# Kernel tuning notes

Measured on AMD Instinct MI355X. Metric: run time of the kernel, lower is better.

Reference implementation:

```python
import jax, jax.numpy as jnp
import numpy as np

ALPHA = 4.0  # spikingjelly default Sigmoid surrogate alpha
BN_EPS = 1e-5

@jax.custom_vjp
def spike(x):
    return (x >= 0.0).astype(x.dtype)

def _spike_fwd(x):
    return spike(x), x

def _spike_bwd(res, g):
    s = jax.nn.sigmoid(ALPHA * res)
    return (g * ALPHA * s * (1.0 - s),)

spike.defvjp(_spike_fwd, _spike_bwd)

def lif(x, tau=2.0, vth=1.0):
    # MultiStepLIFNode: hard reset (v_reset=0), detach_reset=True, scan over time axis 0
    def step(v, xt):
        h = v + (xt - v) / tau          # charge
        s = spike(h - vth)              # fire (surrogate grad)
        v_next = h * (1.0 - jax.lax.stop_gradient(s))  # detached hard reset to 0
        return v_next, s
    _, out = jax.lax.scan(step, jnp.zeros_like(x[0]), x)
    return out

def conv_bn(x, w, b, g, be, m, var):
    # x: [TB, C, N]; 1x1 Conv1d is a channel GEMM, then eval-mode BatchNorm1d
    y = jnp.einsum('oc,bcn->bon', w, x) + b[None, :, None]
    inv = g / jnp.sqrt(var + BN_EPS)
    return (y - m[None, :, None]) * inv[None, :, None] + be[None, :, None]

def setup_inputs() -> dict:
    key = jax.random.key(0)
    T, B, C, H, W = 4, 32, 512, 14, 14
    ks = jax.random.split(key, 32)
    d = {'x': jax.random.normal(ks[0], (T, B, C, H, W), dtype=jnp.float32)}
    scale = 1.0 / np.sqrt(C)
    i = 1
    for p in ['q', 'k', 'v', 'p']:
        d[p + '_cw'] = jax.random.normal(ks[i], (C, C), dtype=jnp.float32) * scale; i += 1
        d[p + '_cb'] = jax.random.normal(ks[i], (C,), dtype=jnp.float32) * 0.1; i += 1
        d[p + '_bg'] = jnp.ones((C,), dtype=jnp.float32)
        d[p + '_bb'] = jnp.zeros((C,), dtype=jnp.float32)
        d[p + '_bm'] = jax.random.normal(ks[i], (C,), dtype=jnp.float32) * 0.1; i += 1
        d[p + '_bv'] = jax.random.uniform(ks[i], (C,), dtype=jnp.float32, minval=0.5, maxval=1.5); i += 1
    d['push_w'] = jnp.asarray(1.0, dtype=jnp.float32)
    d['pull_w'] = jnp.asarray(1.0, dtype=jnp.float32)
    d['pp_bias'] = jnp.asarray(0.0, dtype=jnp.float32)
    return d

def reference(x,
              q_cw, q_cb, q_bg, q_bb, q_bm, q_bv,
              k_cw, k_cb, k_bg, k_bb, k_bm, k_bv,
              v_cw, v_cb, v_bg, v_bb, v_bm, v_bv,
              p_cw, p_cb, p_bg, p_bb, p_bm, p_bv,
              push_w, pull_w, pp_bias):
    T, B, C, H, W = x.shape
    N = H * W
    nh = 8
    hd = C // nh
    scale = 0.125

    xs = lif(x)                                   # head_lif, [T,B,C,H,W]
    xf = xs.reshape(T * B, C, N)
    q = conv_bn(xf, q_cw, q_cb, q_bg, q_bb, q_bm, q_bv).reshape(T, B, C, N)
    k = conv_bn(xf, k_cw, k_cb, k_bg, k_bb, k_bm, k_bv).reshape(T, B, C, N)
    v = conv_bn(xf, v_cw, v_cb, v_bg, v_bb, v_bm, v_bv).reshape(T, B, C, N)

    q_on = lif(q)
    q_off = lif(-q)

    def to_heads(t):  # [T,B,C,N] -> [T,B,nh,N,hd]
        return jnp.swapaxes(t, -1, -2).reshape(T, B, N, nh, hd).transpose(0, 1, 3, 2, 4)

    q_on_h = to_heads(q_on)
    q_off_h = to_heads(q_off)
    k_h = to_heads(lif(k))
    v_h = to_heads(lif(v))

    pw = jax.nn.softplus(push_w)
    pl = jax.nn.softplus(pull_w)
    diff = pw * q_on_h - pl * q_off_h + pp_bias   # push-pull gating
    q_pp = lif(diff)

    kv = jnp.einsum('tbhnd,tbhne->tbhde', k_h, v_h)      # k^T @ v, [T,B,h,hd,hd]
    o = jnp.einsum('tbhnd,tbhde->tbhne', q_pp, kv) * scale

    o = o.transpose(0, 1, 2, 4, 3).reshape(T, B, C, N)   # transpose(3,4) then merge heads
    o = lif(o, vth=0.5)                                   # attn_lif
    o = conv_bn(o.reshape(T * B, C, N), p_cw, p_cb, p_bg, p_bb, p_bm, p_bv)
    return o.reshape(T, B, C, H, W)
```

## Files before the change

kernel.cpp:

```cpp
#include <hip/hip_runtime.h>
#include <hip/hip_bf16.h>
#include <math.h>

typedef unsigned short u16;
typedef unsigned int   u32;

#define CC 512
#define NN 196
#define TT 4
#define BB 32
#define TBB 128
#define NHH 8
#define HD 64

#define ROWS_T  6272
#define CSTRIDE ((size_t)ROWS_T * CC)

typedef __attribute__((ext_vector_type(8))) _Float16 f16x8;
typedef __attribute__((ext_vector_type(4))) float f32x4;

#define ONE_H 0x3C00

__device__ __forceinline__ u16 h_bits(_Float16 h) { return *(u16*)&h; }
__device__ __forceinline__ float h2f(u16 u) { return (float)(*(const _Float16*)&u); }
__device__ __forceinline__ u32 pk2(u16 a, u16 b) { return (u32)a | ((u32)b << 16); }

__device__ __forceinline__ void gld16(const void* g, void* l) {
    __builtin_amdgcn_global_load_lds(
        (const __attribute__((address_space(1))) void*)g,
        (__attribute__((address_space(3))) void*)l, 16, 0, 0);
}

__global__ __launch_bounds__(256) void k_prep(
    const float* __restrict__ qw, const float* __restrict__ kw,
    const float* __restrict__ vw, const float* __restrict__ pw,
    const float* __restrict__ cb0, const float* __restrict__ bg0, const float* __restrict__ bb0,
    const float* __restrict__ bm0, const float* __restrict__ bv0,
    const float* __restrict__ cb1, const float* __restrict__ bg1, const float* __restrict__ bb1,
    const float* __restrict__ bm1, const float* __restrict__ bv1,
    const float* __restrict__ cb2, const float* __restrict__ bg2, const float* __restrict__ bb2,
    const float* __restrict__ bm2, const float* __restrict__ bv2,
    const float* __restrict__ cb3, const float* __restrict__ bg3, const float* __restrict__ bb3,
    const float* __restrict__ bm3, const float* __restrict__ bv3,
    u16* __restrict__ W2, float* __restrict__ SS, float* __restrict__ SH) {
    if (blockIdx.x < 4096) {
        size_t idx = (size_t)blockIdx.x * 256 + threadIdx.x;
        int g = (int)(idx >> 18);
        size_t rem = idx & 262143;
        const float* Ws = (g == 0) ? qw : (g == 1) ? kw : (g == 2) ? vw : pw;
        float w  = Ws[rem];
        _Float16 h0 = (fabsf(w) < 6.2e-5f) ? (_Float16)0.0f : (_Float16)w;
        float r = (w - (float)h0) * 2048.0f;
        _Float16 h1 = (_Float16)r;
        size_t base = (size_t)g * 524288 + rem;
        W2[base] = h_bits(h0); W2[base + 262144] = h_bits(h1);
        return;
    }
    int idx = (blockIdx.x - 4096) * 256 + threadIdx.x;
    int g = idx >> 9, o = idx & 511;
    const float* cb = g == 0 ? cb0 : g == 1 ? cb1 : g == 2 ? cb2 : cb3;
    const float* bg = g == 0 ? bg0 : g == 1 ? bg1 : g == 2 ? bg2 : bg3;
    const float* bb = g == 0 ? bb0 : g == 1 ? bb1 : g == 2 ? bb2 : bb3;
    const float* bm = g == 0 ? bm0 : g == 1 ? bm1 : g == 2 ? bm2 : bm3;
    const float* bv = g == 0 ? bv0 : g == 1 ? bv1 : g == 2 ? bv2 : bv3;
    float inv = bg[o] / sqrtf(bv[o] + 1e-5f);
    SS[g * 512 + o] = inv;
    SH[g * 512 + o] = (cb[o] - bm[o]) * inv + bb[o];
}

__global__ __launch_bounds__(256) void k_head_lif(const float* __restrict__ x, u16* __restrict__ XS) {
    __shared__ float T[64][65];
    const int tid = threadIdx.x;
    const int n0 = blockIdx.x * 64;
    const int b  = blockIdx.y;
    const int c_base = blockIdx.z * 64;
    const int c_l = tid >> 4;
    const int n4  = (tid & 15) * 4;
    const bool lv = (n0 + n4) < NN;
    const int n_r = tid >> 2;
    const int cq  = (tid & 3) * 16;
    const bool wv = (n0 + n_r) < NN;

    float v[4][4];
    #pragma unroll
    for (int k = 0; k < 4; ++k)
        #pragma unroll
        for (int j = 0; j < 4; ++j) v[k][j] = 0.f;

    for (int t = 0; t < TT; ++t) {
        const size_t xb = ((size_t)(t * BB + b) * CC + c_base) * NN;
        float s[4][4];
        #pragma unroll
        for (int k = 0; k < 4; ++k) {
            const int c = c_l + 16 * k;
            float4 xv = make_float4(0.f, 0.f, 0.f, 0.f);
            if (lv) xv = *(const float4*)(x + xb + (size_t)c * NN + n0 + n4);
            float xa[4] = {xv.x, xv.y, xv.z, xv.w};
            #pragma unroll
            for (int j = 0; j < 4; ++j) {
                float h = v[k][j] + (xa[j] - v[k][j]) * 0.5f;
                s[k][j] = (h >= 1.f) ? 1.f : 0.f;
                v[k][j] = (h >= 1.f) ? 0.f : h;
            }
        }
        __syncthreads();
        #pragma unroll
        for (int k = 0; k < 4; ++k)
            #pragma unroll
            for (int j = 0; j < 4; ++j) T[c_l + 16 * k][n4 + j] = s[k][j];
        __syncthreads();
        if (wv) {
            const size_t ob = ((size_t)(t * BB + b) * NN + n0 + n_r) * CC + c_base + cq;
            u16 u[16];
            #pragma unroll
            for (int m = 0; m < 16; ++m) u[m] = (T[cq + m][n_r] != 0.f) ? ONE_H : 0;
            uint4 q0 = make_uint4(pk2(u[0],u[1]),  pk2(u[2],u[3]),  pk2(u[4],u[5]),  pk2(u[6],u[7]));
            uint4 q1 = make_uint4(pk2(u[8],u[9]),  pk2(u[10],u[11]),pk2(u[12],u[13]),pk2(u[14],u[15]));
            *(uint4*)(XS + ob)     = q0;
            *(uint4*)(XS + ob + 8) = q1;
        }
        __syncthreads();
    }
}

__global__ __launch_bounds__(256) void k_gemm_qkv(const u16* __restrict__ S, const u16* __restrict__ W2,
                                                  const float* __restrict__ scale, const float* __restrict__ shift,
                                                  u16* __restrict__ QS, u16* __restrict__ KS, u16* __restrict__ VS,
                                                  const float* __restrict__ PW, const float* __restrict__ PL,
                                                  const float* __restrict__ PB) {
    __shared__ __align__(16) u16 smem[24576];
    u16* Xt  = smem;
    u16* WtF = smem + 8192;
    const int tid  = threadIdx.x;
    const int lane = tid & 63;
    const int w    = tid >> 6;
    const int bid  = blockIdx.x;
    const int work = (bid & 7) * 294 + (bid >> 3);
    const int rrt  = work / 12;
    const int gw   = work - rrt * 12;
    const int g    = gw >> 2;
    const int wtile = gw & 3;
    const int rr0  = rrt * 32;
    const u16* Wb = W2 + (size_t)g * 524288 + (size_t)(wtile * 128) * CC;
    const float* scl = scale + g * 512;
    const float* shf = shift + g * 512;

    const int lrow8  = lane >> 3;
    const int gchunk = ((lane & 7) ^ lrow8) * 8;
    const int l15 = lane & 15;
    const int q4  = lane >> 4;
    const int wm = (w >> 1) * 64, wn = (w & 1) * 64;

    const size_t arow0 = (size_t)w * CSTRIDE + (size_t)rr0 * CC;

    f32x4 acc[4][4];
    f32x4 zz = {0.f, 0.f, 0.f, 0.f};
    #pragma unroll
    for (int i = 0; i < 4; ++i)
        #pragma unroll
        for (int j = 0; j < 4; ++j) acc[i][j] = zz;

    for (int c0 = 0; c0 < CC; c0 += 64) {
        __syncthreads();
        #pragma unroll
        for (int i = 0; i < 4; ++i) {
            int p = w * 4 + i;
            gld16(S + arow0 + (size_t)(i * 8 + lrow8) * CC + c0 + gchunk, &Xt[p * 512]);
        }
        #pragma unroll
        for (int i = 0; i < 8; ++i) {
            int lin = w * 8 + i;
            int s = lin >> 4, p = lin & 15;
            gld16(Wb + (size_t)s * 262144 + (size_t)(p * 8 + lrow8) * CC + c0 + gchunk,
                  WtF + s * 8192 + p * 512);
        }
        __syncthreads();

        #pragma unroll
        for (int ks = 0; ks < 2; ++ks) {
            const int cpo = ((ks * 4 + q4) ^ (l15 & 7)) * 8;
            f16x8 sf[4], sflo[4];
            #pragma unroll
            for (int i = 0; i < 4; ++i) {
                sf[i]   = *(const f16x8*)&Xt[(wm + i * 16 + l15) * 64 + cpo];
                sflo[i] = sf[i] * (_Float16)0.00048828125f;
            }
            #pragma unroll
            for (int s = 0; s < 2; ++s) {
                f16x8 wf[4];
                #pragma unroll
                for (int i = 0; i < 4; ++i)
                    wf[i] = *(const f16x8*)&WtF[s * 8192 + (wn + i * 16 + l15) * 64 + cpo];
                #pragma unroll
                for (int mt = 0; mt < 4; ++mt)
                    #pragma unroll
                    for (int nt = 0; nt < 4; ++nt)
                        acc[mt][nt] = __builtin_amdgcn_mfma_f32_16x16x32_f16(
                            s ? sflo[mt] : sf[mt], wf[nt], acc[mt][nt], 0, 0, 0);
            }
        }
    }

    const float pwv = (g == 0) ? log1pf(expf(PW[0])) : 0.f;
    const float plv = (g == 0) ? log1pf(expf(PL[0])) : 0.f;
    const float pbv = (g == 0) ? PB[0] : 0.f;
    u16* OUT = (g == 0) ? QS : (g == 1) ? KS : VS;
    float* LY = (float*)smem;
    const int pairid = w & 1;
    const int pr  = tid >> 7;
    const int idx = tid & 127;

    #pragma unroll
    for (int cc = 0; cc < 2; ++cc) {
        __syncthreads();
        #pragma unroll
        for (int ntl = 0; ntl < 2; ++ntl) {
            const int nt = cc * 2 + ntl;
            const int o  = wtile * 128 + wn + nt * 16 + l15;
            const float sc = scl[o], sh = shf[o];
            const int col32 = ntl * 16 + l15;
            #pragma unroll
            for (int mt = 0; mt < 4; ++mt) {
                const int tr0 = wm + mt * 16 + q4 * 4;
                #pragma unroll
                for (int r = 0; r < 4; ++r)
                    LY[(pairid * 128 + tr0 + r) * 33 + col32] = acc[mt][nt][r] * sc + sh;
            }
        }
        __syncthreads();
        #pragma unroll
        for (int stp = 0; stp < 4; ++stp) {
            const int chain = stp * 128 + idx;
            const int nn  = chain >> 4;
            const int c2  = (chain & 15) * 2;
            const int rr  = rr0 + nn;
            const float* Lp = &LY[(pr * 128 + nn) * 33 + c2];
            float ya[4][2];
            #pragma unroll
            for (int t = 0; t < 4; ++t) {
                ya[t][0] = Lp[t * 32 * 33];
                ya[t][1] = Lp[t * 32 * 33 + 1];
            }
            const int ocol = wtile * 128 + pr * 64 + cc * 32 + c2;
            u32* op = (u32*)(OUT + (size_t)rr * CC + ocol);
            if (g == 0) {
                float von[2] = {0.f, 0.f}, voff[2] = {0.f, 0.f}, vpp[2] = {0.f, 0.f};
                #pragma unroll
                for (int t = 0; t < 4; ++t) {
                    u16 sp2[2];
                    #pragma unroll
                    for (int j = 0; j < 2; ++j) {
                        float qv = ya[t][j], h;
                        h = von[j]  + ( qv - von[j] ) * 0.5f; bool s1 = (h >= 1.f); von[j]  = s1 ? 0.f : h;
                        h = voff[j] + (-qv - voff[j]) * 0.5f; bool s2 = (h >= 1.f); voff[j] = s2 ? 0.f : h;
                        float diff = pwv * (s1 ? 1.f : 0.f) - plv * (s2 ? 1.f : 0.f) + pbv;
                        h = vpp[j] + (diff - vpp[j]) * 0.5f; bool sp = (h >= 1.f); vpp[j] = sp ? 0.f : h;
                        sp2[j] = sp ? ONE_H : 0;
                    }
                    op[t * (CSTRIDE / 2)] = pk2(sp2[0], sp2[1]);
                }
            } else {
                float vm[2] = {0.f, 0.f};
                #pragma unroll
                for (int t = 0; t < 4; ++t) {
                    u16 s2[2];
                    #pragma unroll
                    for (int j = 0; j < 2; ++j) {
                        float h = vm[j] + (ya[t][j] - vm[j]) * 0.5f;
                        bool s = (h >= 1.f); vm[j] = s ? 0.f : h;
                        s2[j] = s ? ONE_H : 0;
                    }
                    op[t * (CSTRIDE / 2)] = pk2(s2[0], s2[1]);
                }
            }
        }
    }
}

__global__ __launch_bounds__(256) void k_attn(const u16* __restrict__ Q, const u16* __restrict__ K,
                                              const u16* __restrict__ V, u16* __restrict__ OS) {
    __shared__ __align__(16) u16 sm[19584];
    u16* Kt  = sm;
    u16* Vt  = sm + 8704;
    u16* Qs  = sm;
    u16* kvT = sm + 14976;

    const int tid = threadIdx.x;
    const int tb  = blockIdx.x >> 3;
    const int h   = blockIdx.x & 7;
    const size_t gb = (size_t)tb * NN * CC + (size_t)h * HD;

    const int srow = tid >> 2;
    const int sdq  = (tid & 3) * 16;

    const int lane = tid & 63;
    const int w    = tid >> 6;
    const int l15  = lane & 15;
    const int kb8  = (lane >> 4) * 8;
    const int quad = (lane >> 4) * 4;
    const int dh = (w >> 1) * 32, eh = (w & 1) * 32;

    f32x4 accA[2][2];
    f32x4 zz = {0.f, 0.f, 0.f, 0.f};
    #pragma unroll
    for (int i = 0; i < 2; ++i)
        #pragma unroll
        for (int j = 0; j < 2; ++j) accA[i][j] = zz;

    const uint4 z4 = make_uint4(0, 0, 0, 0);

    #pragma unroll
    for (int ch = 0; ch < 2; ++ch) {
        if (ch) __syncthreads();
        #pragma unroll
        for (int c = 0; c < 2; ++c) {
            int n  = ch * 128 + c * 64 + srow;
            int nl = c * 64 + srow;
            bool valid = n < NN;
            const u16* kr = K + gb + (size_t)n * CC + sdq;
            const u16* vr = V + gb + (size_t)n * CC + sdq;
            uint4 ka  = valid ? *(const uint4*)kr : z4;
            uint4 kb2 = valid ? *(const uint4*)(kr + 8) : z4;
            uint4 va  = valid ? *(const uint4*)vr : z4;
            uint4 vb2 = valid ? *(const uint4*)(vr + 8) : z4;
            u32 kwv[8] = {ka.x, ka.y, ka.z, ka.w, kb2.x, kb2.y, kb2.z, kb2.w};
            u32 vwv[8] = {va.x, va.y, va.z, va.w, vb2.x, vb2.y, vb2.z, vb2.w};
            #pragma unroll
            for (int i = 0; i < 8; ++i) {
                Kt[(sdq + 2 * i) * 136 + nl]     = (u16)(kwv[i] & 0xFFFF);
                Kt[(sdq + 2 * i + 1) * 136 + nl] = (u16)(kwv[i] >> 16);
                Vt[(sdq + 2 * i) * 136 + nl]     = (u16)(vwv[i] & 0xFFFF);
                Vt[(sdq + 2 * i + 1) * 136 + nl] = (u16)(vwv[i] >> 16);
            }
        }
        __syncthreads();
        #pragma unroll
        for (int k0 = 0; k0 < 128; k0 += 32) {
            f16x8 af[2], bv[2];
            #pragma unroll
            for (int i = 0; i < 2; ++i) {
                af[i] = *(const f16x8*)&Kt[(dh + i * 16 + l15) * 136 + k0 + kb8];
                bv[i] = *(const f16x8*)&Vt[(eh + i * 16 + l15) * 136 + k0 + kb8];
            }
            #pragma unroll
            for (int i = 0; i < 2; ++i)
                #pragma unroll
                for (int j = 0; j < 2; ++j)
                    accA[i][j] = __builtin_amdgcn_mfma_f32_16x16x32_f16(af[i], bv[j], accA[i][j], 0, 0, 0);
        }
    }
    __syncthreads();

    #pragma unroll
    for (int i = 0; i < 2; ++i)
        #pragma unroll
        for (int j = 0; j < 2; ++j)
            #pragma unroll
            for (int r = 0; r < 4; ++r) {
                int e = eh + j * 16 + l15;
                int d = dh + i * 16 + quad + r;
                _Float16 hv = (_Float16)accA[i][j][r];
                kvT[e * 72 + d] = h_bits(hv);
            }
    #pragma unroll
    for (int p = 0; p < 4; ++p) {
        int n = p * 64 + srow;
        if (n < 208) {
            if (n < NN) {
                const u16* qr = Q + gb + (size_t)n * CC + sdq;
                uint4 qa  = *(const uint4*)qr;
                uint4 qb2 = *(const uint4*)(qr + 8);
                u32 qwv[8] = {qa.x, qa.y, qa.z, qa.w, qb2.x, qb2.y, qb2.z, qb2.w};
                #pragma unroll
                for (int i = 0; i < 8; ++i) {
                    Qs[n * 72 + sdq + 2 * i]     = (u16)(qwv[i] & 0xFFFF);
                    Qs[n * 72 + sdq + 2 * i + 1] = (u16)(qwv[i] >> 16);
                }
            } else {
                #pragma unroll
                for (int i = 0; i < 16; ++i) Qs[n * 72 + sdq + i] = 0;
            }
        }
    }
    __syncthreads();

    f16x8 bq0 = *(const f16x8*)&kvT[(w * 16 + l15) * 72 + 0  + kb8];
    f16x8 bq1 = *(const f16x8*)&kvT[(w * 16 + l15) * 72 + 32 + kb8];
    u16* ob = OS + (size_t)tb * NN * CC + (size_t)h * HD + w * 16 + l15;
    #pragma unroll
    for (int nt = 0; nt < 13; ++nt) {
        f32x4 acc = zz;
        f16x8 a0 = *(const f16x8*)&Qs[(nt * 16 + l15) * 72 + 0  + kb8];
        f16x8 a1 = *(const f16x8*)&Qs[(nt * 16 + l15) * 72 + 32 + kb8];
        acc = __builtin_amdgcn_mfma_f32_16x16x32_f16(a0, bq0, acc, 0, 0, 0);
        acc = __builtin_amdgcn_mfma_f32_16x16x32_f16(a1, bq1, acc, 0, 0, 0);
        #pragma unroll
        for (int r = 0; r < 4; ++r) {
            int n = nt * 16 + quad + r;
            if (n < NN) {
                _Float16 ov = (_Float16)(acc[r] * 0.125f);
                ob[(size_t)n * CC] = h_bits(ov);
            }
        }
    }
}

__global__ __launch_bounds__(256) void k_attn_lif(uint4* __restrict__ OS) {
    const size_t idx = (size_t)blockIdx.x * 256 + threadIdx.x;
    float v[8];
    #pragma unroll
    for (int j = 0; j < 8; ++j) v[j] = 0.f;
    #pragma unroll
    for (int t = 0; t < TT; ++t) {
        const size_t o8 = idx + (size_t)t * (CSTRIDE / 8);
        uint4 d = OS[o8];
        u32 dw[4] = {d.x, d.y, d.z, d.w};
        u16 u[8];
        #pragma unroll
        for (int p = 0; p < 4; ++p) {
            #pragma unroll
            for (int hf = 0; hf < 2; ++hf) {
                int j = p * 2 + hf;
                u16 raw = hf ? (u16)(dw[p] >> 16) : (u16)(dw[p] & 0xFFFF);
                float xv = h2f(raw);
                float h = v[j] + (xv - v[j]) * 0.5f;
                bool s = (h >= 0.5f);
                v[j] = s ? 0.f : h;
                u[j] = s ? ONE_H : 0;
            }
        }
        OS[o8] = make_uint4(pk2(u[0],u[1]), pk2(u[2],u[3]), pk2(u[4],u[5]), pk2(u[6],u[7]));
    }
}

__global__ __launch_bounds__(256) void k_gemm_proj(const u16* __restrict__ S, const u16* __restrict__ W2,
                                                   const float* __restrict__ scale, const float* __restrict__ shift,
                                                   float* __restrict__ Y) {
    __shared__ __align__(16) u16 Xt[128 * 64];
    __shared__ __align__(16) u16 Wt[2][128 * 64];
    const int tid  = threadIdx.x;
    const int lane = tid & 63;
    const int w    = tid >> 6;
    const int bid  = blockIdx.x;
    const int work = (bid & 7) * 98 + (bid >> 3);
    const int ntile = work >> 2;
    const int wtile = work & 3;
    const u16* Sb = S + (size_t)ntile * 128 * CC;
    const u16* Wb = W2 + (size_t)(wtile * 128) * CC;

    const int lrow8  = lane >> 3;
    const int gchunk = ((lane & 7) ^ lrow8) * 8;
    const int l15 = lane & 15;
    const int q4  = lane >> 4;
    const int wm = (w >> 1) * 64, wn = (w & 1) * 64;

    const int tb0 = (ntile * 128) / NN;
    const int bnd = (tb0 + 1) * NN;

    f32x4 acc[4][4];
    f32x4 zz = {0.f, 0.f, 0.f, 0.f};
    #pragma unroll
    for (int i = 0; i < 4; ++i)
        #pragma unroll
        for (int j = 0; j < 4; ++j) acc[i][j] = zz;

    for (int c0 = 0; c0 < CC; c0 += 64) {
        __syncthreads();
        #pragma unroll
        for (int i = 0; i < 4; ++i) {
            int p = w * 4 + i;
            gld16(Sb + (size_t)(p * 8 + lrow8) * CC + c0 + gchunk, &Xt[p * 512]);
        }
        #pragma unroll
        for (int i = 0; i < 8; ++i) {
            int lin = w * 8 + i;
            int s = lin >> 4, p = lin & 15;
            gld16(Wb + (size_t)s * 262144 + (size_t)(p * 8 + lrow8) * CC + c0 + gchunk,
                  &Wt[s][p * 512]);
        }
        __syncthreads();

        #pragma unroll
        for (int ks = 0; ks < 2; ++ks) {
            const int cpo = ((ks * 4 + q4) ^ (l15 & 7)) * 8;
            f16x8 sf[4], sflo[4];
            #pragma unroll
            for (int i = 0; i < 4; ++i) {
                sf[i]   = *(const f16x8*)&Xt[(wn + i * 16 + l15) * 64 + cpo];
                sflo[i] = sf[i] * (_Float16)0.00048828125f;
            }
            #pragma unroll
            for (int s = 0; s < 2; ++s) {
                f16x8 wf[4];
                #pragma unroll
                for (int i = 0; i < 4; ++i)
                    wf[i] = *(const f16x8*)&Wt[s][(wm + i * 16 + l15) * 64 + cpo];
                #pragma unroll
                for (int mt = 0; mt < 4; ++mt)
                    #pragma unroll
                    for (int nt = 0; nt < 4; ++nt)
                        acc[mt][nt] = __builtin_amdgcn_mfma_f32_16x16x32_f16(
                            wf[mt], s ? sflo[nt] : sf[nt], acc[mt][nt], 0, 0, 0);
            }
        }
    }

    #pragma unroll
    for (int mt = 0; mt < 4; ++mt) {
        int o0 = wtile * 128 + wm + mt * 16 + (lane >> 4) * 4;
        #pragma unroll
        for (int nt = 0; nt < 4; ++nt) {
            int row = ntile * 128 + wn + nt * 16 + l15;
            int tb = (row >= bnd) ? tb0 + 1 : tb0;
            int n  = row - tb * NN;
            #pragma unroll
            for (int r = 0; r < 4; ++r)
                Y[((size_t)tb * CC + o0 + r) * NN + n] = acc[mt][nt][r] * scale[o0 + r] + shift[o0 + r];
        }
    }
}

extern "C" void kernel_launch(void* const* d_in, const int* in_sizes, int n_in,
                              void* d_out, int out_size, void* d_ws, size_t ws_size,
                              hipStream_t stream) {
    const float* x    = (const float*)d_in[0];
    const float* q_cw = (const float*)d_in[1];
    const float* q_cb = (const float*)d_in[2];
    const float* q_bg = (const float*)d_in[3];
    const float* q_bb = (const float*)d_in[4];
    const float* q_bm = (const float*)d_in[5];
    const float* q_bv = (const float*)d_in[6];
    const float* k_cw = (const float*)d_in[7];
    const float* k_cb = (const float*)d_in[8];
    const float* k_bg = (const float*)d_in[9];
    const float* k_bb = (const float*)d_in[10];
    const float* k_bm = (const float*)d_in[11];
    const float* k_bv = (const float*)d_in[12];
    const float* v_cw = (const float*)d_in[13];
    const float* v_cb = (const float*)d_in[14];
    const float* v_bg = (const float*)d_in[15];
    const float* v_bb = (const float*)d_in[16];
    const float* v_bm = (const float*)d_in[17];
    const float* v_bv = (const float*)d_in[18];
    const float* p_cw = (const float*)d_in[19];
    const float* p_cb = (const float*)d_in[20];
    const float* p_bg = (const float*)d_in[21];
    const float* p_bb = (const float*)d_in[22];
    const float* p_bm = (const float*)d_in[23];
    const float* p_bv = (const float*)d_in[24];
    const float* pshw = (const float*)d_in[25];
    const float* pllw = (const float*)d_in[26];
    const float* ppb  = (const float*)d_in[27];
    float* out = (float*)d_out;

    if (ws_size < (size_t)242 * 1024 * 1024) return;
    char* W = (char*)d_ws;
    u16*   XS = (u16*)W;
    u16*   QS = (u16*)(W + ((size_t)27 << 20));
    u16*   OS = (u16*)(W + ((size_t)78 << 20));
    u16*   KS = (u16*)(W + ((size_t)182 << 20));
    u16*   VS = (u16*)(W + ((size_t)208 << 20));
    u16*   W2 = (u16*)(W + ((size_t)234 << 20));
    float* SS = (float*)(W + ((size_t)238 << 20));
    float* SH = SS + 2048;

    k_prep<<<4104, 256, 0, stream>>>(q_cw, k_cw, v_cw, p_cw,
                                     q_cb, q_bg, q_bb, q_bm, q_bv,
                                     k_cb, k_bg, k_bb, k_bm, k_bv,
                                     v_cb, v_bg, v_bb, v_bm, v_bv,
                                     p_cb, p_bg, p_bb, p_bm, p_bv, W2, SS, SH);

    k_head_lif<<<dim3(4, 32, 8), 256, 0, stream>>>(x, XS);

    k_gemm_qkv<<<2352, 256, 0, stream>>>(XS, W2, SS, SH, QS, KS, VS, pshw, pllw, ppb);

    k_attn<<<TBB * NHH, 256, 0, stream>>>(QS, KS, VS, OS);
    k_attn_lif<<<1568, 256, 0, stream>>>((uint4*)OS);

    k_gemm_proj<<<784, 256, 0, stream>>>(OS, W2 + 3 * 524288, SS + 1536, SH + 1536, out);
}
```

Baseline: 321.6 us.

## Merge prep and head LIF launches, swizzle K/V LDS tiles, vectorize LDS stores

Merges the weight/BN preparation kernel and the head LIF kernel into one launch by dispatching on block index, which removes one launch and lets the two independent jobs share the GPU. In the attention kernel, the padded K/V transpose tiles are replaced by an XOR-swizzled unpadded layout to cut LDS bank conflicts. The kv tile and Q staging writes are vectorized into packed 64-bit stores instead of 16-bit scalar stores. The fused kernel now always reserves the head LIF shared buffer, which may lower occupancy for the prep blocks.

```diff
diff --git a/kernel.cpp b/kernel.cpp
--- a/kernel.cpp
+++ b/kernel.cpp
@@ -31,7 +31,8 @@
         (__attribute__((address_space(3))) void*)l, 16, 0, 0);
 }
 
-__global__ __launch_bounds__(256) void k_prep(
+__global__ __launch_bounds__(256) void k_prep_head(
+    const float* __restrict__ x, u16* __restrict__ XS,
     const float* __restrict__ qw, const float* __restrict__ kw,
     const float* __restrict__ vw, const float* __restrict__ pw,
     const float* __restrict__ cb0, const float* __restrict__ bg0, const float* __restrict__ bb0,
@@ -43,8 +44,11 @@
     const float* __restrict__ cb3, const float* __restrict__ bg3, const float* __restrict__ bb3,
     const float* __restrict__ bm3, const float* __restrict__ bv3,
     u16* __restrict__ W2, float* __restrict__ SS, float* __restrict__ SH) {
+    __shared__ float T[64][65];
+    const int tid = threadIdx.x;
+
     if (blockIdx.x < 4096) {
-        size_t idx = (size_t)blockIdx.x * 256 + threadIdx.x;
+        size_t idx = (size_t)blockIdx.x * 256 + tid;
         int g = (int)(idx >> 18);
         size_t rem = idx & 262143;
         const float* Ws = (g == 0) ? qw : (g == 1) ? kw : (g == 2) ? vw : pw;
@@ -56,24 +60,24 @@
         W2[base] = h_bits(h0); W2[base + 262144] = h_bits(h1);
         return;
     }
-    int idx = (blockIdx.x - 4096) * 256 + threadIdx.x;
-    int g = idx >> 9, o = idx & 511;
-    const float* cb = g == 0 ? cb0 : g == 1 ? cb1 : g == 2 ? cb2 : cb3;
-    const float* bg = g == 0 ? bg0 : g == 1 ? bg1 : g == 2 ? bg2 : bg3;
-    const float* bb = g == 0 ? bb0 : g == 1 ? bb1 : g == 2 ? bb2 : bb3;
-    const float* bm = g == 0 ? bm0 : g == 1 ? bm1 : g == 2 ? bm2 : bm3;
-    const float* bv = g == 0 ? bv0 : g == 1 ? bv1 : g == 2 ? bv2 : bv3;
-    float inv = bg[o] / sqrtf(bv[o] + 1e-5f);
-    SS[g * 512 + o] = inv;
-    SH[g * 512 + o] = (cb[o] - bm[o]) * inv + bb[o];
-}
-
-__global__ __launch_bounds__(256) void k_head_lif(const float* __restrict__ x, u16* __restrict__ XS) {
-    __shared__ float T[64][65];
-    const int tid = threadIdx.x;
-    const int n0 = blockIdx.x * 64;
-    const int b  = blockIdx.y;
-    const int c_base = blockIdx.z * 64;
+    if (blockIdx.x < 4104) {
+        int idx = (blockIdx.x - 4096) * 256 + tid;
+        int g = idx >> 9, o = idx & 511;
+        const float* cb = g == 0 ? cb0 : g == 1 ? cb1 : g == 2 ? cb2 : cb3;
+        const float* bg = g == 0 ? bg0 : g == 1 ? bg1 : g == 2 ? bg2 : bg3;
+        const float* bb = g == 0 ? bb0 : g == 1 ? bb1 : g == 2 ? bb2 : bb3;
+        const float* bm = g == 0 ? bm0 : g == 1 ? bm1 : g == 2 ? bm2 : bm3;
+        const float* bv = g == 0 ? bv0 : g == 1 ? bv1 : g == 2 ? bv2 : bv3;
+        float inv = bg[o] / sqrtf(bv[o] + 1e-5f);
+        SS[g * 512 + o] = inv;
+        SH[g * 512 + o] = (cb[o] - bm[o]) * inv + bb[o];
+        return;
+    }
+
+    const int hidx = blockIdx.x - 4104;
+    const int n0 = (hidx & 3) * 64;
+    const int b  = (hidx >> 2) & 31;
+    const int c_base = (hidx >> 7) * 64;
     const int c_l = tid >> 4;
     const int n4  = (tid & 15) * 4;
     const bool lv = (n0 + n4) < NN;
@@ -281,7 +285,7 @@
                                               const u16* __restrict__ V, u16* __restrict__ OS) {
     __shared__ __align__(16) u16 sm[19584];
     u16* Kt  = sm;
-    u16* Vt  = sm + 8704;
+    u16* Vt  = sm + 8192;
     u16* Qs  = sm;
     u16* kvT = sm + 14976;
 
@@ -316,6 +320,7 @@
         for (int c = 0; c < 2; ++c) {
             int n  = ch * 128 + c * 64 + srow;
             int nl = c * 64 + srow;
+            const int nch = nl >> 3, noff = nl & 7;
             bool valid = n < NN;
             const u16* kr = K + gb + (size_t)n * CC + sdq;
             const u16* vr = V + gb + (size_t)n * CC + sdq;
@@ -327,10 +332,14 @@
             u32 vwv[8] = {va.x, va.y, va.z, va.w, vb2.x, vb2.y, vb2.z, vb2.w};
             #pragma unroll
             for (int i = 0; i < 8; ++i) {
-                Kt[(sdq + 2 * i) * 136 + nl]     = (u16)(kwv[i] & 0xFFFF);
-                Kt[(sdq + 2 * i + 1) * 136 + nl] = (u16)(kwv[i] >> 16);
-                Vt[(sdq + 2 * i) * 136 + nl]     = (u16)(vwv[i] & 0xFFFF);
-                Vt[(sdq + 2 * i + 1) * 136 + nl] = (u16)(vwv[i] >> 16);
+                const int row0 = sdq + 2 * i;
+                const int x0 = (row0 ^ (row0 >> 3)) & 7;
+                const int cb0 = ((nch ^ x0) << 3) + noff;
+                const int cb1 = ((nch ^ x0 ^ 1) << 3) + noff;
+                Kt[row0 * 128 + cb0]       = (u16)(kwv[i] & 0xFFFF);
+                Kt[(row0 + 1) * 128 + cb1] = (u16)(kwv[i] >> 16);
+                Vt[row0 * 128 + cb0]       = (u16)(vwv[i] & 0xFFFF);
+                Vt[(row0 + 1) * 128 + cb1] = (u16)(vwv[i] >> 16);
             }
         }
         __syncthreads();
@@ -339,8 +348,13 @@
             f16x8 af[2], bv[2];
             #pragma unroll
             for (int i = 0; i < 2; ++i) {
-                af[i] = *(const f16x8*)&Kt[(dh + i * 16 + l15) * 136 + k0 + kb8];
-                bv[i] = *(const f16x8*)&Vt[(eh + i * 16 + l15) * 136 + k0 + kb8];
+                const int rowa = dh + i * 16 + l15;
+                const int xa = (rowa ^ (rowa >> 3)) & 7;
+                const int rowb = eh + i * 16 + l15;
+                const int xb = (rowb ^ (rowb >> 3)) & 7;
+                const int chnk = (k0 + kb8) >> 3;
+                af[i] = *(const f16x8*)&Kt[rowa * 128 + ((chnk ^ xa) << 3)];
+                bv[i] = *(const f16x8*)&Vt[rowb * 128 + ((chnk ^ xb) << 3)];
             }
             #pragma unroll
             for (int i = 0; i < 2; ++i)
@@ -354,31 +368,32 @@
     #pragma unroll
     for (int i = 0; i < 2; ++i)
         #pragma unroll
-        for (int j = 0; j < 2; ++j)
-            #pragma unroll
-            for (int r = 0; r < 4; ++r) {
-                int e = eh + j * 16 + l15;
-                int d = dh + i * 16 + quad + r;
-                _Float16 hv = (_Float16)accA[i][j][r];
-                kvT[e * 72 + d] = h_bits(hv);
-            }
+        for (int j = 0; j < 2; ++j) {
+            const int e  = eh + j * 16 + l15;
+            const int d0 = dh + i * 16 + quad;
+            _Float16 h0 = (_Float16)accA[i][j][0];
+            _Float16 h1 = (_Float16)accA[i][j][1];
+            _Float16 h2 = (_Float16)accA[i][j][2];
+            _Float16 h3 = (_Float16)accA[i][j][3];
+            uint2 wv = make_uint2(pk2(h_bits(h0), h_bits(h1)), pk2(h_bits(h2), h_bits(h3)));
+            *(uint2*)&kvT[e * 72 + d0] = wv;
+        }
     #pragma unroll
     for (int p = 0; p < 4; ++p) {
         int n = p * 64 + srow;
         if (n < 208) {
+            uint2* qp = (uint2*)&Qs[n * 72 + sdq];
             if (n < NN) {
                 const u16* qr = Q + gb + (size_t)n * CC + sdq;
                 uint4 qa  = *(const uint4*)qr;
                 uint4 qb2 = *(const uint4*)(qr + 8);
-                u32 qwv[8] = {qa.x, qa.y, qa.z, qa.w, qb2.x, qb2.y, qb2.z, qb2.w};
-                #pragma unroll
-                for (int i = 0; i < 8; ++i) {
-                    Qs[n * 72 + sdq + 2 * i]     = (u16)(qwv[i] & 0xFFFF);
-                    Qs[n * 72 + sdq + 2 * i + 1] = (u16)(qwv[i] >> 16);
-                }
+                qp[0] = make_uint2(qa.x, qa.y);
+                qp[1] = make_uint2(qa.z, qa.w);
+                qp[2] = make_uint2(qb2.x, qb2.y);
+                qp[3] = make_uint2(qb2.z, qb2.w);
             } else {
-                #pragma unroll
-                for (int i = 0; i < 16; ++i) Qs[n * 72 + sdq + i] = 0;
+                uint2 z2 = make_uint2(0, 0);
+                qp[0] = z2; qp[1] = z2; qp[2] = z2; qp[3] = z2;
             }
         }
     }
@@ -564,13 +579,12 @@
     float* SS = (float*)(W + ((size_t)238 << 20));
     float* SH = SS + 2048;
 
-    k_prep<<<4104, 256, 0, stream>>>(q_cw, k_cw, v_cw, p_cw,
-                                     q_cb, q_bg, q_bb, q_bm, q_bv,
-                                     k_cb, k_bg, k_bb, k_bm, k_bv,
-                                     v_cb, v_bg, v_bb, v_bm, v_bv,
-                                     p_cb, p_bg, p_bb, p_bm, p_bv, W2, SS, SH);
-
-    k_head_lif<<<dim3(4, 32, 8), 256, 0, stream>>>(x, XS);
+    k_prep_head<<<5128, 256, 0, stream>>>(x, XS,
+                                          q_cw, k_cw, v_cw, p_cw,
+                                          q_cb, q_bg, q_bb, q_bm, q_bv,
+                                          k_cb, k_bg, k_bb, k_bm, k_bv,
+                                          v_cb, v_bg, v_bb, v_bm, v_bv,
+                                          p_cb, p_bg, p_bb, p_bm, p_bv, W2, SS, SH);
 
     k_gemm_qkv<<<2352, 256, 0, stream>>>(XS, W2, SS, SH, QS, KS, VS, pshw, pllw, ppb);
 
```

Result: slower. 328.9 us (+2.3%).
